# Optimization experiments

Hardware: AMD Instinct MI355X
Metric: run time of the kernel (lower is better)

Reference implementation:

```python
import jax, jax.numpy as jnp
import numpy as np

DIM = 256
HEADS = 8
HEAD_DIM = DIM // HEADS
WS = 7            # window size
SHIFT = 3         # shift size
H = 56
W = 56
B = 32
WA = WS * WS      # window area = 49
NWH, NWW = H // WS, W // WS
NW = NWH * NWW    # windows per image


def _make_attn_mask():
    # replicate the torch mask construction for the shifted windows
    img = np.zeros((H, W), dtype=np.float32)
    cnt = 0
    for hs in (slice(0, -WS), slice(-WS, -SHIFT), slice(-SHIFT, None)):
        for ws_ in (slice(0, -WS), slice(-WS, -SHIFT), slice(-SHIFT, None)):
            img[hs, ws_] = cnt
            cnt += 1
    mw = img.reshape(NWH, WS, NWW, WS).transpose(0, 2, 1, 3).reshape(-1, WA)  # (nW, 49)
    diff = mw[:, None, :] - mw[:, :, None]                                    # (nW, 49, 49)
    return np.where(diff != 0, -100.0, 0.0).astype(np.float32)


def _make_rel_index():
    coords = np.stack(np.meshgrid(np.arange(WS), np.arange(WS), indexing='ij')).reshape(2, -1)
    rel = coords[:, :, None] - coords[:, None, :]        # (2, 49, 49)
    rel = rel.transpose(1, 2, 0) + (WS - 1)              # shift to >= 0
    rel[..., 0] *= 2 * WS - 1
    return rel.sum(-1).astype(np.int32)                  # (49, 49) in [0, 169)


def setup_inputs() -> dict:
    key = jax.random.key(0)
    ks = jax.random.split(key, 12)
    s = 0.02
    inp = {
        'x': jax.random.normal(ks[0], (B, H, W, DIM), dtype=jnp.float32),
        'ln1_w': jnp.ones((DIM,), jnp.float32), 'ln1_b': jnp.zeros((DIM,), jnp.float32),
        'qkv_w': s * jax.random.normal(ks[1], (3 * DIM, DIM), jnp.float32),
        'qkv_b': jnp.zeros((3 * DIM,), jnp.float32),
        'rpb_table': s * jax.random.normal(ks[2], ((2 * WS - 1) ** 2, HEADS), jnp.float32),
        'proj_w': s * jax.random.normal(ks[3], (DIM, DIM), jnp.float32),
        'proj_b': jnp.zeros((DIM,), jnp.float32),
        'ln2_w': jnp.ones((DIM,), jnp.float32), 'ln2_b': jnp.zeros((DIM,), jnp.float32),
        'fc1_w': s * jax.random.normal(ks[4], (4 * DIM, DIM), jnp.float32),
        'fc1_b': jnp.zeros((4 * DIM,), jnp.float32),
        'ln3_w': jnp.ones((4 * DIM,), jnp.float32), 'ln3_b': jnp.zeros((4 * DIM,), jnp.float32),
        'fc2_w': s * jax.random.normal(ks[5], (DIM, 4 * DIM), jnp.float32),
        'fc2_b': jnp.zeros((DIM,), jnp.float32),
        'attn_mask': jnp.asarray(_make_attn_mask()),     # (nW, 49, 49)
        'rel_index': jnp.asarray(_make_rel_index()),     # (49, 49) int32
    }
    return inp


def _ln(x, w, b, eps=1e-5):
    m = jnp.mean(x, axis=-1, keepdims=True)
    v = jnp.mean((x - m) ** 2, axis=-1, keepdims=True)
    return (x - m) * jax.lax.rsqrt(v + eps) * w + b


def reference(x, ln1_w, ln1_b, qkv_w, qkv_b, rpb_table, proj_w, proj_b,
              ln2_w, ln2_b, fc1_w, fc1_b, ln3_w, ln3_b, fc2_w, fc2_b,
              attn_mask, rel_index):
    Bn, Hn, Wn, C = x.shape
    # ---- attention branch ----
    y = _ln(x, ln1_w, ln1_b)
    sh = jnp.roll(y, (-SHIFT, -SHIFT), axis=(1, 2))
    # window partition: (B, H, W, C) -> (B*nW, 49, C)
    win = sh.reshape(Bn, NWH, WS, NWW, WS, C).transpose(0, 1, 3, 2, 4, 5).reshape(Bn * NW, WA, C)
    qkv = win @ qkv_w.T + qkv_b                              # (Bw, 49, 3C)
    qkv = qkv.reshape(Bn * NW, WA, 3, HEADS, HEAD_DIM).transpose(2, 0, 3, 1, 4)
    q, k, v = qkv[0], qkv[1], qkv[2]                         # (Bw, h, 49, d)
    scale = HEAD_DIM ** -0.5
    attn = jnp.einsum('bhqd,bhkd->bhqk', q * scale, k)       # (Bw, h, 49, 49)
    bias = rpb_table[rel_index]                              # (49, 49, h)
    attn = attn + jnp.transpose(bias, (2, 0, 1))[None]
    attn = attn.reshape(Bn, NW, HEADS, WA, WA) + attn_mask[None, :, None]
    attn = jax.nn.softmax(attn, axis=-1).reshape(Bn * NW, HEADS, WA, WA)
    out = jnp.einsum('bhqk,bhkd->bhqd', attn, v)             # (Bw, h, 49, d)
    out = out.transpose(0, 2, 1, 3).reshape(Bn * NW, WA, C)
    out = out @ proj_w.T + proj_b
    # window reverse + un-shift
    out = out.reshape(Bn, NWH, NWW, WS, WS, C).transpose(0, 1, 3, 2, 4, 5).reshape(Bn, Hn, Wn, C)
    out = jnp.roll(out, (SHIFT, SHIFT), axis=(1, 2))
    x = x + out
    # ---- MLP branch (note: extra LayerNorm inside MLP per source) ----
    z = _ln(x, ln2_w, ln2_b)
    h = jax.nn.gelu(z @ fc1_w.T + fc1_b, approximate=False)
    h = _ln(h, ln3_w, ln3_b)
    x = x + (h @ fc2_w.T + fc2_b)
    return x
```

## Files before the change

### kernel.cpp

```cpp
#include <hip/hip_runtime.h>
#include <hip/hip_bf16.h>
#include <math.h>

typedef __attribute__((ext_vector_type(8))) short bf16x8;
typedef __attribute__((ext_vector_type(4))) float f32x4;
typedef __attribute__((ext_vector_type(4))) float f4;
typedef __attribute__((ext_vector_type(8))) unsigned short us8;
typedef __attribute__((ext_vector_type(4))) unsigned short us4;
typedef unsigned short u16;
typedef unsigned int u32;

#define HEADS 8
#define SHIFT_ 3
#define HIMG 56
#define WIMG 56
#define WA 49
#define NTOK 100352
#define NPAIR 16384

static __device__ __forceinline__ float bf2f(u16 v){ return __uint_as_float(((u32)v)<<16); }
static __device__ __forceinline__ u16 f2bf(float f){
  u32 u = __float_as_uint(f);
  return (u16)((u + 0x7fffu + ((u>>16)&1u)) >> 16);
}
static __device__ __forceinline__ float wsum(float v){
  #pragma unroll
  for (int off=32; off>0; off>>=1) v += __shfl_xor(v, off, 64);
  return v;
}
static __device__ __forceinline__ void glds16(const u16* g, u16* l){
  __builtin_amdgcn_global_load_lds(
      (const __attribute__((address_space(1))) unsigned int*)g,
      (__attribute__((address_space(3))) unsigned int*)l, 16, 0, 0);
}
static __device__ __forceinline__ int tok2pix(int row){
  int bw = row / 49, t = row - bw*49;
  int b  = bw >> 6,  w = bw & 63;
  int wh = w >> 3,   ww = w & 7;
  int th = t / 7,    tw = t - th*7;
  int r = wh*7 + th + SHIFT_; if (r >= HIMG) r -= HIMG;
  int c = ww*7 + tw + SHIFT_; if (c >= WIMG) c -= WIMG;
  return (b*HIMG + r)*WIMG + c;
}
static __device__ __forceinline__ float gelu_f(float x){
  float x2 = x*x;
  float u  = x*(0.7978845608028654f + 0.0356774081363001f*x2);
  float e  = __expf(u+u);
  float th = 1.0f - 2.0f*__builtin_amdgcn_rcpf(1.0f+e);
  return 0.5f*x*(1.0f+th);
}

__global__ void zero_kernel(float* __restrict__ p){
  p[blockIdx.x*256 + threadIdx.x] = 0.f;
}

template<int C, int ISBF>
__global__ void ln_stats_kernel(const void* __restrict__ srcv, float* __restrict__ stats){
  int wave = threadIdx.x >> 6, lane = threadIdx.x & 63;
  int tok = blockIdx.x*4 + wave;
  float s=0.f, s2=0.f;
  if (ISBF == 0){
    const float* p = (const float*)srcv + (size_t)tok*C;
    #pragma unroll
    for (int i=0;i<C/256;i++){
      f4 v = *(const f4*)(p + lane*4*(C/256) + i*4);
      #pragma unroll
      for (int e=0;e<4;e++){ float f=v[e]; s+=f; s2+=f*f; }
    }
  } else {
    const u16* p = (const u16*)srcv + (size_t)tok*C;
    #pragma unroll
    for (int i=0;i<C/512;i++){
      us8 v = *(const us8*)(p + lane*8*(C/512) + i*8);
      #pragma unroll
      for (int e=0;e<8;e++){ float f=bf2f(v[e]); s+=f; s2+=f*f; }
    }
  }
  s = wsum(s); s2 = wsum(s2);
  if (lane==0){
    float mean = s/(float)C;
    float var  = s2/(float)C - mean*mean;
    stats[2*tok]   = mean;
    stats[2*tok+1] = rsqrtf(var + 1e-5f);
  }
}

__global__ void ln_apply_kernel(const float* __restrict__ src, u16* __restrict__ dst){
  int wave = threadIdx.x >> 6, lane = threadIdx.x & 63;
  int tok = blockIdx.x*4 + wave;
  const float* p = src + (size_t)tok*256;
  f4 a = *(const f4*)(p + lane*4);
  float s = a[0]+a[1]+a[2]+a[3];
  float s2 = a[0]*a[0]+a[1]*a[1]+a[2]*a[2]+a[3]*a[3];
  s = wsum(s); s2 = wsum(s2);
  float mean = s*(1.f/256.f);
  float var  = s2*(1.f/256.f) - mean*mean;
  float rstd = rsqrtf(var + 1e-5f);
  us4 o;
  #pragma unroll
  for (int e=0;e<4;e++) o[e] = f2bf((a[e]-mean)*rstd);
  *(us4*)(dst + (size_t)tok*256 + lane*4) = o;
}

__global__ void prep_weights(
    const float* __restrict__ qkv_w, const float* __restrict__ qkv_b,
    const float* __restrict__ ln1w,  const float* __restrict__ ln1b,
    const float* __restrict__ fc1_w, const float* __restrict__ fc1_b,
    const float* __restrict__ ln2w,  const float* __restrict__ ln2b,
    const float* __restrict__ fc2_w, const float* __restrict__ fc2_b,
    const float* __restrict__ ln3w,  const float* __restrict__ ln3b,
    const float* __restrict__ proj_w, const float* __restrict__ proj_b,
    u16* __restrict__ wq, float* __restrict__ bq,
    u16* __restrict__ w1, float* __restrict__ b1,
    u16* __restrict__ w2, float* __restrict__ b2,
    u16* __restrict__ wp, float* __restrict__ bp,
    float* __restrict__ cs2)
{
  int wave = threadIdx.x>>6, lane = threadIdx.x&63;
  int n = blockIdx.x*4 + wave;
  const float *W,*lw,*lb,*bs; u16* WO; float* BO; int K, row, noln, docs;
  if (n < 768)      { W=qkv_w; lw=ln1w; lb=ln1b; bs=qkv_b; WO=wq; BO=bq; K=256;  row=n;      noln=0; docs=0; }
  else if (n < 1792){ W=fc1_w; lw=ln2w; lb=ln2b; bs=fc1_b; WO=w1; BO=b1; K=256;  row=n-768;  noln=0; docs=0; }
  else if (n < 2048){ W=fc2_w; lw=ln3w; lb=ln3b; bs=fc2_b; WO=w2; BO=b2; K=1024; row=n-1792; noln=0; docs=1; }
  else              { W=proj_w; lw=nullptr; lb=nullptr; bs=proj_b; WO=wp; BO=bp; K=256; row=n-2048; noln=1; docs=0; }
  float dot = 0.f, cs = 0.f;
  for (int k=lane; k<K; k+=64){
    float wv = W[(size_t)row*K + k];
    if (noln){
      WO[(size_t)row*K + k] = f2bf(wv);
    } else {
      dot += wv * lb[k];
      u16 q = f2bf(wv * lw[k]);
      WO[(size_t)row*K + k] = q;
      cs += bf2f(q);
    }
  }
  dot = wsum(dot);
  if (docs){ cs = wsum(cs); if (lane==0) cs2[row] = cs; }
  if (lane==0) BO[row] = bs[row] + dot;
}

template<int SMODE, int EPI, int SWAP>
__global__ __launch_bounds__(256)
void gemm8(const void* __restrict__ Av, const u16* __restrict__ Bt,
           const float* __restrict__ stats, float* __restrict__ hstats,
           const float* __restrict__ biasf, const float* __restrict__ resid,
           const float* __restrict__ colsum, void* __restrict__ outv,
           int K, int NT, int CHUNK)
{
  constexpr int BM=128, BN=128, BK=64;
  __shared__ u16 smem[16384];
  u16* As = smem;
  u16* Bs = smem + 8192;
  int b = blockIdx.x;
  int linear = (b & 7)*CHUNK + (b >> 3);
  int mt = linear / NT, nt = linear - mt*NT;
  int m0 = mt*BM, n0 = nt*BN;
  int tid  = threadIdx.x;
  int lane = tid & 63, wave = tid >> 6;
  int wr = wave >> 1, wc = wave & 1;
  int lc16 = lane & 15, g = lane >> 4;
  int nsteps = K >> 6;

  const u16* asrc[4];
  const u16* bsrc[4];
  #pragma unroll
  for (int i=0;i<4;i++){
    int c = tid + i*256;
    int row = c >> 3, ch = (c & 7) ^ (row & 7);
    if (SMODE <= 1){
      int grow = (SMODE==0) ? tok2pix(m0+row) : (m0+row);
      asrc[i] = (const u16*)Av + (size_t)grow*K + ch*8;
    }
    bsrc[i] = Bt + (size_t)(n0+row)*K + ch*8;
  }
  float smean[4], srstd[4];
  if (SMODE == 3){
    #pragma unroll
    for (int i=0;i<4;i++){
      int grow = m0 + ((tid + i*256) >> 3);
      smean[i] = stats[2*grow]; srstd[i] = stats[2*grow+1];
    }
  }

  f32x4 acc[4][4];
  #pragma unroll
  for (int i=0;i<4;i++)
    #pragma unroll
    for (int j=0;j<4;j++){ acc[i][j][0]=0.f; acc[i][j][1]=0.f; acc[i][j][2]=0.f; acc[i][j][3]=0.f; }

  f4 rcurf[4][2];
  if (SMODE == 3){
    #pragma unroll
    for (int i=0;i<4;i++){
      int c = tid + i*256; int row = c>>3, ch = c&7;
      const float* ap = (const float*)Av + (size_t)(m0+row)*K + ch*8;
      rcurf[i][0] = *(const f4*)ap; rcurf[i][1] = *(const f4*)(ap+4);
    }
  }

  for (int t=0; t<nsteps; ++t){
    int kt = t << 6;
    if (SMODE <= 1){
      #pragma unroll
      for (int i=0;i<4;i++) glds16(asrc[i]+kt, As + i*2048 + wave*512);
    } else {
      #pragma unroll
      for (int i=0;i<4;i++){
        int c = tid + i*256; int row = c>>3, ch = c&7;
        us8 o;
        #pragma unroll
        for (int e=0;e<8;e++){
          float fv = rcurf[i][e>>2][e&3];
          o[e] = f2bf((fv - smean[i])*srstd[i]);
        }
        u32 byte = (u32)(row*128 + ch*16) ^ ((u32)(row&7)<<4);
        *(us8*)(As + (byte>>1)) = o;
      }
    }
    #pragma unroll
    for (int i=0;i<4;i++) glds16(bsrc[i]+kt, Bs + i*2048 + wave*512);
    __syncthreads();
    if (SMODE == 3 && t+1 < nsteps){
      int kt1 = kt + 64;
      f4 rnextf[4][2];
      #pragma unroll
      for (int i=0;i<4;i++){
        int c = tid + i*256; int row = c>>3, ch = c&7;
        const float* ap = (const float*)Av + (size_t)(m0+row)*K + kt1 + ch*8;
        rnextf[i][0] = *(const f4*)ap; rnextf[i][1] = *(const f4*)(ap+4);
      }
      #pragma unroll
      for (int kk=0; kk<2; kk++){
        bf16x8 af[4], bfr[4];
        #pragma unroll
        for (int mi=0;mi<4;mi++){
          int r = wr*64 + mi*16 + lc16;
          u32 byte = (u32)(r*128 + kk*64 + g*16) ^ ((u32)(r&7)<<4);
          af[mi] = *(const bf16x8*)(As + (byte>>1));
        }
        #pragma unroll
        for (int ni=0;ni<4;ni++){
          int r = wc*64 + ni*16 + lc16;
          u32 byte = (u32)(r*128 + kk*64 + g*16) ^ ((u32)(r&7)<<4);
          bfr[ni] = *(const bf16x8*)(Bs + (byte>>1));
        }
        #pragma unroll
        for (int mi=0;mi<4;mi++)
          #pragma unroll
          for (int ni=0;ni<4;ni++)
            acc[mi][ni] = SWAP ? __builtin_amdgcn_mfma_f32_16x16x32_bf16(bfr[ni], af[mi], acc[mi][ni], 0, 0, 0)
                               : __builtin_amdgcn_mfma_f32_16x16x32_bf16(af[mi], bfr[ni], acc[mi][ni], 0, 0, 0);
      }
      #pragma unroll
      for (int i=0;i<4;i++){ rcurf[i][0] = rnextf[i][0]; rcurf[i][1] = rnextf[i][1]; }
    } else {
      #pragma unroll
      for (int kk=0; kk<2; kk++){
        bf16x8 af[4], bfr[4];
        #pragma unroll
        for (int mi=0;mi<4;mi++){
          int r = wr*64 + mi*16 + lc16;
          u32 byte = (u32)(r*128 + kk*64 + g*16) ^ ((u32)(r&7)<<4);
          af[mi] = *(const bf16x8*)(As + (byte>>1));
        }
        #pragma unroll
        for (int ni=0;ni<4;ni++){
          int r = wc*64 + ni*16 + lc16;
          u32 byte = (u32)(r*128 + kk*64 + g*16) ^ ((u32)(r&7)<<4);
          bfr[ni] = *(const bf16x8*)(Bs + (byte>>1));
        }
        #pragma unroll
        for (int mi=0;mi<4;mi++)
          #pragma unroll
          for (int ni=0;ni<4;ni++)
            acc[mi][ni] = SWAP ? __builtin_amdgcn_mfma_f32_16x16x32_bf16(bfr[ni], af[mi], acc[mi][ni], 0, 0, 0)
                               : __builtin_amdgcn_mfma_f32_16x16x32_bf16(af[mi], bfr[ni], acc[mi][ni], 0, 0, 0);
      }
    }
    __syncthreads();
  }

  int lr = lane >> 4;
  if (EPI==0){
    u16* Cs = smem;
    #pragma unroll
    for (int mi=0;mi<4;mi++){
      #pragma unroll
      for (int ni=0;ni<4;ni++){
        int cl = wc*64 + ni*16 + lc16;
        float bv = biasf[n0 + cl];
        #pragma unroll
        for (int j=0;j<4;j++){
          int rl = wr*64 + mi*16 + lr*4 + j;
          float v = acc[mi][ni][j] + bv;
          u32 byte = (u32)(rl*256 + cl*2) ^ ((u32)(rl&7)<<4);
          Cs[byte>>1] = f2bf(v);
        }
      }
    }
    __syncthreads();
    #pragma unroll
    for (int i=0;i<8;i++){
      int c = tid + i*256;
      int rl = c>>4, c0 = (c&15)*8;
      u32 byte = (u32)(rl*256 + c0*2) ^ ((u32)(rl&7)<<4);
      us8 v = *(const us8*)(Cs + (byte>>1));
      int row = m0 + rl, col = n0 + c0;
      int which = col>>8, hh = (col>>5)&7, d0 = col&31;
      int bwi = row/49, t = row - bwi*49;
      *(us8*)((u16*)outv + ((size_t)which*NPAIR + bwi*8 + hh)*(WA*32) + t*32 + d0) = v;
    }
  } else if (EPI==2){
    u16* Cs = smem;
    #pragma unroll
    for (int mi=0;mi<4;mi++){
      int rl = wr*64 + mi*16 + lc16;
      float ss = 0.f, sq = 0.f;
      #pragma unroll
      for (int ni=0;ni<4;ni++){
        int cl = wc*64 + ni*16 + g*4;
        f4 bv = *(const f4*)(biasf + n0 + cl);
        us4 o;
        #pragma unroll
        for (int j=0;j<4;j++){
          float v = gelu_f(acc[mi][ni][j] + bv[j]);
          ss += v; sq += v*v;
          o[j] = f2bf(v);
        }
        u32 byte = (u32)(rl*256 + cl*2) ^ ((u32)(rl&7)<<4);
        *(us4*)(Cs + (byte>>1)) = o;
      }
      ss += __shfl_xor(ss, 16, 64); ss += __shfl_xor(ss, 32, 64);
      sq += __shfl_xor(sq, 16, 64); sq += __shfl_xor(sq, 32, 64);
      if (g==0){
        int grow = m0 + rl;
        atomicAdd(&hstats[2*grow],   ss);
        atomicAdd(&hstats[2*grow+1], sq);
      }
    }
    __syncthreads();
    #pragma unroll
    for (int i=0;i<8;i++){
      int c = tid + i*256;
      int rl = c>>4, c0 = (c&15)*8;
      u32 byte = (u32)(rl*256 + c0*2) ^ ((u32)(rl&7)<<4);
      us8 v = *(const us8*)(Cs + (byte>>1));
      int row = m0 + rl, col = n0 + c0;
      *(us8*)((u16*)outv + (size_t)row*1024 + col) = v;
    }
  } else {
    float* Cs = (float*)smem;
    #pragma unroll
    for (int hp=0; hp<2; hp++){
      if (hp) __syncthreads();
      if (wc == hp){
        #pragma unroll
        for (int mi=0;mi<4;mi++){
          float rs4[4], mr4[4];
          if (EPI==4){
            #pragma unroll
            for (int j=0;j<4;j++){
              int grow = m0 + wr*64 + mi*16 + lr*4 + j;
              float s = stats[2*grow], q = stats[2*grow+1];
              float mean = s*(1.f/1024.f);
              float var  = q*(1.f/1024.f) - mean*mean;
              rs4[j] = rsqrtf(var + 1e-5f);
              mr4[j] = mean*rs4[j];
            }
          }
          #pragma unroll
          for (int ni=0;ni<4;ni++){
            int cl = ni*16 + lc16;
            int col = n0 + hp*64 + cl;
            float bv = biasf[col];
            float cw = (EPI==4) ? colsum[col] : 0.f;
            #pragma unroll
            for (int j=0;j<4;j++){
              int rl = wr*64 + mi*16 + lr*4 + j;
              float v;
              if (EPI==4) v = acc[mi][ni][j]*rs4[j] - mr4[j]*cw + bv;
              else        v = acc[mi][ni][j] + bv;
              u32 byte = (u32)(rl*256 + cl*4) ^ ((u32)(rl&7)<<4);
              *(float*)((char*)Cs + byte) = v;
            }
          }
        }
      }
      __syncthreads();
      #pragma unroll
      for (int i=0;i<8;i++){
        int c = tid + i*256;
        int row = c>>4, ch = c&15;
        u32 byte = (u32)(row*256 + ch*16) ^ ((u32)(row&7)<<4);
        f4 v = *(const f4*)((const char*)Cs + byte);
        int grow = m0 + row, col = n0 + hp*64 + ch*4;
        size_t addr;
        if (EPI==1) addr = (size_t)tok2pix(grow)*256 + col;
        else        addr = (size_t)grow*256 + col;
        f4 rr = *(const f4*)(resid + addr);
        v += rr;
        *(f4*)((float*)outv + addr) = v;
      }
    }
  }
}

__global__ void attn_mfma_kernel(
    const u16* __restrict__ qkv,
    const float* __restrict__ rpb,
    const int* __restrict__ rel,
    const float* __restrict__ mask,
    u16* __restrict__ outb)
{
  __shared__ u16 Kls[4][64*32];
  __shared__ u16 Vt [4][32*64];
  __shared__ u16 Pls[4][64*64];
  int wave = threadIdx.x>>6, lane = threadIdx.x&63;
  int pair = blockIdx.x*4 + wave;
  int bw = pair>>3, h = pair&7, w = bw&63;
  int lc = lane&15, g = lane>>4;
  const u16* qg = qkv + (size_t)pair*(WA*32);
  const u16* kg = qg + (size_t)NPAIR*(WA*32);
  const u16* vg = qg + (size_t)2*NPAIR*(WA*32);
  u16* Kp = &Kls[wave][0];
  u16* Vp = &Vt[wave][0];
  u16* Pp = &Pls[wave][0];

  #pragma unroll
  for (int i=0;i<4;i++){
    int idx = i*64 + lane;
    int r = idx>>2, seg = idx&3;
    us8 kv, vv;
    if (r < WA){
      kv = *(const us8*)(kg + r*32 + seg*8);
      vv = *(const us8*)(vg + r*32 + seg*8);
    } else {
      #pragma unroll
      for (int e=0;e<8;e++){ kv[e]=0; vv[e]=0; }
    }
    *(us8*)(Kp + r*32 + seg*8) = kv;
    #pragma unroll
    for (int e=0;e<8;e++){
      int d = seg*8 + e;
      u32 byte = ((u32)(d*128 + r*2)) ^ ((u32)(d&7)<<4);
      Vp[byte>>1] = vv[e];
    }
  }

  bf16x8 qa[4];
  #pragma unroll
  for (int mi=0;mi<4;mi++){
    int r = mi*16 + lc;
    if (r < WA) qa[mi] = *(const bf16x8*)(qg + r*32 + g*8);
    else { bf16x8 z;
           #pragma unroll
           for (int e=0;e<8;e++) z[e]=0; qa[mi]=z; }
  }

  f32x4 acc[4][4];
  #pragma unroll
  for (int i=0;i<4;i++)
    #pragma unroll
    for (int j=0;j<4;j++){ acc[i][j][0]=0.f; acc[i][j][1]=0.f; acc[i][j][2]=0.f; acc[i][j][3]=0.f; }
  __syncthreads();
  #pragma unroll
  for (int ni=0;ni<4;ni++){
    bf16x8 kb = *(const bf16x8*)(Kp + (ni*16+lc)*32 + g*8);
    #pragma unroll
    for (int mi=0;mi<4;mi++)
      acc[mi][ni] = __builtin_amdgcn_mfma_f32_16x16x32_bf16(qa[mi], kb, acc[mi][ni], 0, 0, 0);
  }

  const float scale = 0.17677669529663689f;
  float rinv[4][4];
  #pragma unroll
  for (int mi=0;mi<4;mi++){
    #pragma unroll
    for (int jr=0;jr<4;jr++){
      int i = mi*16 + g*4 + jr;
      float sv[4];
      #pragma unroll
      for (int ni=0;ni<4;ni++){
        int j = ni*16 + lc;
        float s;
        if (i < WA && j < WA){
          s = acc[mi][ni][jr]*scale + rpb[rel[i*WA+j]*8 + h] + mask[((size_t)w*WA + i)*WA + j];
        } else s = -1e9f;
        sv[ni] = s;
      }
      float mx = fmaxf(fmaxf(sv[0],sv[1]), fmaxf(sv[2],sv[3]));
      #pragma unroll
      for (int off=1; off<16; off<<=1) mx = fmaxf(mx, __shfl_xor(mx, off, 64));
      float sum = 0.f;
      #pragma unroll
      for (int ni=0;ni<4;ni++){ sv[ni] = __expf(sv[ni]-mx); sum += sv[ni]; }
      #pragma unroll
      for (int off=1; off<16; off<<=1) sum += __shfl_xor(sum, off, 64);
      rinv[mi][jr] = __builtin_amdgcn_rcpf(sum);
      #pragma unroll
      for (int ni=0;ni<4;ni++){
        int j = ni*16 + lc;
        u32 byte = ((u32)(i*128 + j*2)) ^ ((u32)(i&7)<<4);
        Pp[byte>>1] = f2bf(sv[ni]);
      }
    }
  }

  bf16x8 vb[2][2];
  #pragma unroll
  for (int kk=0;kk<2;kk++)
    #pragma unroll
    for (int ni=0;ni<2;ni++){
      int d = ni*16 + lc;
      u32 byte = ((u32)(d*128 + kk*64 + g*16)) ^ ((u32)(d&7)<<4);
      vb[kk][ni] = *(const bf16x8*)(Vp + (byte>>1));
    }
  f32x4 aco[4][2];
  #pragma unroll
  for (int i=0;i<4;i++)
    #pragma unroll
    for (int j=0;j<2;j++){ aco[i][j][0]=0.f; aco[i][j][1]=0.f; aco[i][j][2]=0.f; aco[i][j][3]=0.f; }
  #pragma unroll
  for (int mi=0;mi<4;mi++){
    int r = mi*16 + lc;
    #pragma unroll
    for (int kk=0;kk<2;kk++){
      u32 byte = ((u32)(r*128 + kk*64 + g*16)) ^ ((u32)(r&7)<<4);
      bf16x8 pa = *(const bf16x8*)(Pp + (byte>>1));
      #pragma unroll
      for (int ni=0;ni<2;ni++)
        aco[mi][ni] = __builtin_amdgcn_mfma_f32_16x16x32_bf16(pa, vb[kk][ni], aco[mi][ni], 0, 0, 0);
    }
  }

  u16* Op = Kp;
  #pragma unroll
  for (int mi=0;mi<4;mi++){
    #pragma unroll
    for (int jr=0;jr<4;jr++){
      int i = mi*16 + g*4 + jr;
      if (i < WA){
        float rv = rinv[mi][jr];
        #pragma unroll
        for (int ni=0;ni<2;ni++)
          Op[i*32 + ni*16 + lc] = f2bf(aco[mi][ni][jr]*rv);
      }
    }
  }
  __syncthreads();
  size_t obase = (size_t)(bw*WA)*256 + h*32;
  #pragma unroll
  for (int i=0;i<4;i++){
    int c = i*64 + lane;
    if (c < WA*4){
      int t = c>>2, seg = c&3;
      *(us8*)(outb + obase + (size_t)t*256 + seg*8) = *(const us8*)(Op + t*32 + seg*8);
    }
  }
}

extern "C" void kernel_launch(void* const* d_in, const int* in_sizes, int n_in,
                              void* d_out, int out_size, void* d_ws, size_t ws_size,
                              hipStream_t stream) {
  const float* x      = (const float*)d_in[0];
  const float* ln1w   = (const float*)d_in[1];
  const float* ln1b   = (const float*)d_in[2];
  const float* qkv_w  = (const float*)d_in[3];
  const float* qkv_b  = (const float*)d_in[4];
  const float* rpb    = (const float*)d_in[5];
  const float* proj_w = (const float*)d_in[6];
  const float* proj_b = (const float*)d_in[7];
  const float* ln2w   = (const float*)d_in[8];
  const float* ln2b   = (const float*)d_in[9];
  const float* fc1_w  = (const float*)d_in[10];
  const float* fc1_b  = (const float*)d_in[11];
  const float* ln3w   = (const float*)d_in[12];
  const float* ln3b   = (const float*)d_in[13];
  const float* fc2_w  = (const float*)d_in[14];
  const float* fc2_b  = (const float*)d_in[15];
  const float* amask  = (const float*)d_in[16];
  const int*   rel    = (const int*)d_in[17];
  float* out = (float*)d_out;

  char* ws = (char*)d_ws;
  float* hstats = (float*)(ws);
  float* statsB = (float*)(ws +  802816);
  float* bq     = (float*)(ws + 1605632);
  float* b1     = (float*)(ws + 1608704);
  float* b2     = (float*)(ws + 1612800);
  float* bp     = (float*)(ws + 1613824);
  float* cs2    = (float*)(ws + 1614848);
  u16*   wq     = (u16*)  (ws + 1615872);
  u16*   w1     = (u16*)  (ws + 2009088);
  u16*   w2     = (u16*)  (ws + 2533376);
  u16*   wp     = (u16*)  (ws + 3057664);
  const size_t P0 = 3188736;
  u16*   qkvbuf = (u16*)(ws + P0);
  u16*   attno  = (u16*)(ws + P0 + 154140672);
  u16*   xb     = (u16*)(ws + P0 + 154140672);
  u16*   hbuf   = (u16*)(ws + P0);
  u16*   x1b    = (u16*)(ws + P0 + 205520896);
  const int bigws = (ws_size >= (size_t)(P0 + 205520896ull + 51380224ull));

  prep_weights<<<576,256,0,stream>>>(qkv_w,qkv_b,ln1w,ln1b, fc1_w,fc1_b,ln2w,ln2b,
                                     fc2_w,fc2_b,ln3w,ln3b, proj_w,proj_b,
                                     wq,bq, w1,b1, w2,b2, wp,bp, cs2);
  ln_apply_kernel<<<NTOK/4,256,0,stream>>>(x, xb);
  gemm8<0,0,0><<<784*6,256,0,stream>>>(xb, wq, nullptr, nullptr, bq, nullptr, nullptr, qkvbuf, 256, 6, 588);
  attn_mfma_kernel<<<NPAIR/4,256,0,stream>>>(qkvbuf, rpb, rel, amask, attno);
  gemm8<1,1,0><<<784*2,256,0,stream>>>(attno, wp, nullptr, nullptr, bp, x, nullptr, out, 256, 2, 196);
  zero_kernel<<<784,256,0,stream>>>(hstats);
  if (bigws){
    ln_apply_kernel<<<NTOK/4,256,0,stream>>>(out, x1b);
    gemm8<1,2,1><<<784*8,256,0,stream>>>(x1b, w1, nullptr, hstats, b1, nullptr, nullptr, hbuf, 256, 8, 784);
  } else {
    ln_stats_kernel<256,0><<<NTOK/4,256,0,stream>>>(out, statsB);
    gemm8<3,2,1><<<784*8,256,0,stream>>>(out, w1, statsB, hstats, b1, nullptr, nullptr, hbuf, 256, 8, 784);
  }
  gemm8<1,4,0><<<784*2,256,0,stream>>>(hbuf, w2, hstats, nullptr, b2, out, cs2, out, 1024, 2, 196);
}
```

Measured before the change: 612.4 us.

## Double-buffer GEMM LDS tiles with BK=32 to overlap global loads

The GEMM kernel's K-step drops from 64 to 32, and the freed LDS is used as two ping-pong buffers for the direct global-to-LDS loads. The next tile's load is issued before the current tile's MFMAs, and each step now has one barrier instead of two. The goal is to hide global load latency behind compute. In exchange the kernel runs twice as many iterations with fewer MFMAs per barrier, and the swizzle moves to a 4-chunk pattern that may raise LDS bank conflicts.

```diff
diff --git a/kernel.cpp b/kernel.cpp
--- a/kernel.cpp
+++ b/kernel.cpp
@@ -142,16 +142,14 @@
 
 template<int SMODE, int EPI, int SWAP>
 __global__ __launch_bounds__(256)
-void gemm8(const void* __restrict__ Av, const u16* __restrict__ Bt,
+void gemm9(const void* __restrict__ Av, const u16* __restrict__ Bt,
            const float* __restrict__ stats, float* __restrict__ hstats,
            const float* __restrict__ biasf, const float* __restrict__ resid,
            const float* __restrict__ colsum, void* __restrict__ outv,
            int K, int NT, int CHUNK)
 {
-  constexpr int BM=128, BN=128, BK=64;
+  constexpr int BM=128, BN=128, BK=32;
   __shared__ u16 smem[16384];
-  u16* As = smem;
-  u16* Bs = smem + 8192;
   int b = blockIdx.x;
   int linear = (b & 7)*CHUNK + (b >> 3);
   int mt = linear / NT, nt = linear - mt*NT;
@@ -160,25 +158,25 @@
   int lane = tid & 63, wave = tid >> 6;
   int wr = wave >> 1, wc = wave & 1;
   int lc16 = lane & 15, g = lane >> 4;
-  int nsteps = K >> 6;
-
-  const u16* asrc[4];
-  const u16* bsrc[4];
-  #pragma unroll
-  for (int i=0;i<4;i++){
+  int nsteps = K >> 5;
+
+  const u16* asrc[2];
+  const u16* bsrc[2];
+  #pragma unroll
+  for (int i=0;i<2;i++){
     int c = tid + i*256;
-    int row = c >> 3, ch = (c & 7) ^ (row & 7);
+    int row = c >> 2, ch = (c & 3) ^ (row & 3);
     if (SMODE <= 1){
       int grow = (SMODE==0) ? tok2pix(m0+row) : (m0+row);
       asrc[i] = (const u16*)Av + (size_t)grow*K + ch*8;
     }
     bsrc[i] = Bt + (size_t)(n0+row)*K + ch*8;
   }
-  float smean[4], srstd[4];
+  float smean[2], srstd[2];
   if (SMODE == 3){
     #pragma unroll
-    for (int i=0;i<4;i++){
-      int grow = m0 + ((tid + i*256) >> 3);
+    for (int i=0;i<2;i++){
+      int grow = m0 + ((tid + i*256) >> 2);
       smean[i] = stats[2*grow]; srstd[i] = stats[2*grow+1];
     }
   }
@@ -189,96 +187,99 @@
     #pragma unroll
     for (int j=0;j<4;j++){ acc[i][j][0]=0.f; acc[i][j][1]=0.f; acc[i][j][2]=0.f; acc[i][j][3]=0.f; }
 
-  f4 rcurf[4][2];
-  if (SMODE == 3){
-    #pragma unroll
-    for (int i=0;i<4;i++){
-      int c = tid + i*256; int row = c>>3, ch = c&7;
+  if (SMODE <= 1){
+    #pragma unroll
+    for (int i=0;i<2;i++) glds16(asrc[i], smem + i*2048 + wave*512);
+    #pragma unroll
+    for (int i=0;i<2;i++) glds16(bsrc[i], smem + 8192 + i*2048 + wave*512);
+    __syncthreads();
+    for (int t=0; t<nsteps; ++t){
+      int cur = t & 1, nxt = cur ^ 1;
+      if (t+1 < nsteps){
+        int kt1 = (t+1) << 5;
+        #pragma unroll
+        for (int i=0;i<2;i++) glds16(asrc[i]+kt1, smem + nxt*4096 + i*2048 + wave*512);
+        #pragma unroll
+        for (int i=0;i<2;i++) glds16(bsrc[i]+kt1, smem + 8192 + nxt*4096 + i*2048 + wave*512);
+      }
+      const u16* Ap = smem + cur*4096;
+      const u16* Bp = smem + 8192 + cur*4096;
+      bf16x8 af[4], bfr[4];
+      #pragma unroll
+      for (int mi=0;mi<4;mi++){
+        int r = wr*64 + mi*16 + lc16;
+        u32 byte = (u32)(r*64 + g*16) ^ ((u32)(r&3)<<4);
+        af[mi] = *(const bf16x8*)(Ap + (byte>>1));
+      }
+      #pragma unroll
+      for (int ni=0;ni<4;ni++){
+        int r = wc*64 + ni*16 + lc16;
+        u32 byte = (u32)(r*64 + g*16) ^ ((u32)(r&3)<<4);
+        bfr[ni] = *(const bf16x8*)(Bp + (byte>>1));
+      }
+      #pragma unroll
+      for (int mi=0;mi<4;mi++)
+        #pragma unroll
+        for (int ni=0;ni<4;ni++)
+          acc[mi][ni] = SWAP ? __builtin_amdgcn_mfma_f32_16x16x32_bf16(bfr[ni], af[mi], acc[mi][ni], 0, 0, 0)
+                             : __builtin_amdgcn_mfma_f32_16x16x32_bf16(af[mi], bfr[ni], acc[mi][ni], 0, 0, 0);
+      __syncthreads();
+    }
+  } else {
+    f4 rcurf[2][2];
+    #pragma unroll
+    for (int i=0;i<2;i++){
+      int c = tid + i*256; int row = c>>2, ch = c&3;
       const float* ap = (const float*)Av + (size_t)(m0+row)*K + ch*8;
       rcurf[i][0] = *(const f4*)ap; rcurf[i][1] = *(const f4*)(ap+4);
     }
-  }
-
-  for (int t=0; t<nsteps; ++t){
-    int kt = t << 6;
-    if (SMODE <= 1){
-      #pragma unroll
-      for (int i=0;i<4;i++) glds16(asrc[i]+kt, As + i*2048 + wave*512);
-    } else {
-      #pragma unroll
-      for (int i=0;i<4;i++){
-        int c = tid + i*256; int row = c>>3, ch = c&7;
+    for (int t=0; t<nsteps; ++t){
+      int kt = t << 5;
+      #pragma unroll
+      for (int i=0;i<2;i++){
+        int c = tid + i*256; int row = c>>2, k8 = (c&3)*8;
         us8 o;
         #pragma unroll
         for (int e=0;e<8;e++){
           float fv = rcurf[i][e>>2][e&3];
           o[e] = f2bf((fv - smean[i])*srstd[i]);
         }
-        u32 byte = (u32)(row*128 + ch*16) ^ ((u32)(row&7)<<4);
-        *(us8*)(As + (byte>>1)) = o;
-      }
-    }
-    #pragma unroll
-    for (int i=0;i<4;i++) glds16(bsrc[i]+kt, Bs + i*2048 + wave*512);
-    __syncthreads();
-    if (SMODE == 3 && t+1 < nsteps){
-      int kt1 = kt + 64;
-      f4 rnextf[4][2];
-      #pragma unroll
-      for (int i=0;i<4;i++){
-        int c = tid + i*256; int row = c>>3, ch = c&7;
-        const float* ap = (const float*)Av + (size_t)(m0+row)*K + kt1 + ch*8;
-        rnextf[i][0] = *(const f4*)ap; rnextf[i][1] = *(const f4*)(ap+4);
-      }
-      #pragma unroll
-      for (int kk=0; kk<2; kk++){
-        bf16x8 af[4], bfr[4];
-        #pragma unroll
-        for (int mi=0;mi<4;mi++){
-          int r = wr*64 + mi*16 + lc16;
-          u32 byte = (u32)(r*128 + kk*64 + g*16) ^ ((u32)(r&7)<<4);
-          af[mi] = *(const bf16x8*)(As + (byte>>1));
+        u32 byte = (u32)(row*64 + k8*2) ^ ((u32)(row&3)<<4);
+        *(us8*)(smem + (byte>>1)) = o;
+      }
+      #pragma unroll
+      for (int i=0;i<2;i++) glds16(bsrc[i]+kt, smem + 8192 + i*2048 + wave*512);
+      __syncthreads();
+      if (t+1 < nsteps){
+        int kt1 = kt + 32;
+        #pragma unroll
+        for (int i=0;i<2;i++){
+          int c = tid + i*256; int row = c>>2, ch = c&3;
+          const float* ap = (const float*)Av + (size_t)(m0+row)*K + kt1 + ch*8;
+          rcurf[i][0] = *(const f4*)ap; rcurf[i][1] = *(const f4*)(ap+4);
         }
-        #pragma unroll
-        for (int ni=0;ni<4;ni++){
-          int r = wc*64 + ni*16 + lc16;
-          u32 byte = (u32)(r*128 + kk*64 + g*16) ^ ((u32)(r&7)<<4);
-          bfr[ni] = *(const bf16x8*)(Bs + (byte>>1));
-        }
-        #pragma unroll
-        for (int mi=0;mi<4;mi++)
-          #pragma unroll
-          for (int ni=0;ni<4;ni++)
-            acc[mi][ni] = SWAP ? __builtin_amdgcn_mfma_f32_16x16x32_bf16(bfr[ni], af[mi], acc[mi][ni], 0, 0, 0)
-                               : __builtin_amdgcn_mfma_f32_16x16x32_bf16(af[mi], bfr[ni], acc[mi][ni], 0, 0, 0);
-      }
-      #pragma unroll
-      for (int i=0;i<4;i++){ rcurf[i][0] = rnextf[i][0]; rcurf[i][1] = rnextf[i][1]; }
-    } else {
-      #pragma unroll
-      for (int kk=0; kk<2; kk++){
-        bf16x8 af[4], bfr[4];
-        #pragma unroll
-        for (int mi=0;mi<4;mi++){
-          int r = wr*64 + mi*16 + lc16;
-          u32 byte = (u32)(r*128 + kk*64 + g*16) ^ ((u32)(r&7)<<4);
-          af[mi] = *(const bf16x8*)(As + (byte>>1));
-        }
-        #pragma unroll
-        for (int ni=0;ni<4;ni++){
-          int r = wc*64 + ni*16 + lc16;
-          u32 byte = (u32)(r*128 + kk*64 + g*16) ^ ((u32)(r&7)<<4);
-          bfr[ni] = *(const bf16x8*)(Bs + (byte>>1));
-        }
-        #pragma unroll
-        for (int mi=0;mi<4;mi++)
-          #pragma unroll
-          for (int ni=0;ni<4;ni++)
-            acc[mi][ni] = SWAP ? __builtin_amdgcn_mfma_f32_16x16x32_bf16(bfr[ni], af[mi], acc[mi][ni], 0, 0, 0)
-                               : __builtin_amdgcn_mfma_f32_16x16x32_bf16(af[mi], bfr[ni], acc[mi][ni], 0, 0, 0);
-      }
-    }
-    __syncthreads();
+      }
+      bf16x8 af[4], bfr[4];
+      #pragma unroll
+      for (int mi=0;mi<4;mi++){
+        int r = wr*64 + mi*16 + lc16;
+        u32 byte = (u32)(r*64 + g*16) ^ ((u32)(r&3)<<4);
+        af[mi] = *(const bf16x8*)(smem + (byte>>1));
+      }
+      #pragma unroll
+      for (int ni=0;ni<4;ni++){
+        int r = wc*64 + ni*16 + lc16;
+        u32 byte = (u32)(r*64 + g*16) ^ ((u32)(r&3)<<4);
+        bfr[ni] = *(const bf16x8*)(smem + 8192 + (byte>>1));
+      }
+      #pragma unroll
+      for (int mi=0;mi<4;mi++)
+        #pragma unroll
+        for (int ni=0;ni<4;ni++)
+          acc[mi][ni] = SWAP ? __builtin_amdgcn_mfma_f32_16x16x32_bf16(bfr[ni], af[mi], acc[mi][ni], 0, 0, 0)
+                             : __builtin_amdgcn_mfma_f32_16x16x32_bf16(af[mi], bfr[ni], acc[mi][ni], 0, 0, 0);
+      __syncthreads();
+    }
   }
 
   int lr = lane >> 4;
@@ -607,16 +608,16 @@
                                      fc2_w,fc2_b,ln3w,ln3b, proj_w,proj_b,
                                      wq,bq, w1,b1, w2,b2, wp,bp, cs2);
   ln_apply_kernel<<<NTOK/4,256,0,stream>>>(x, xb);
-  gemm8<0,0,0><<<784*6,256,0,stream>>>(xb, wq, nullptr, nullptr, bq, nullptr, nullptr, qkvbuf, 256, 6, 588);
+  gemm9<0,0,0><<<784*6,256,0,stream>>>(xb, wq, nullptr, nullptr, bq, nullptr, nullptr, qkvbuf, 256, 6, 588);
   attn_mfma_kernel<<<NPAIR/4,256,0,stream>>>(qkvbuf, rpb, rel, amask, attno);
-  gemm8<1,1,0><<<784*2,256,0,stream>>>(attno, wp, nullptr, nullptr, bp, x, nullptr, out, 256, 2, 196);
+  gemm9<1,1,0><<<784*2,256,0,stream>>>(attno, wp, nullptr, nullptr, bp, x, nullptr, out, 256, 2, 196);
   zero_kernel<<<784,256,0,stream>>>(hstats);
   if (bigws){
     ln_apply_kernel<<<NTOK/4,256,0,stream>>>(out, x1b);
-    gemm8<1,2,1><<<784*8,256,0,stream>>>(x1b, w1, nullptr, hstats, b1, nullptr, nullptr, hbuf, 256, 8, 784);
+    gemm9<1,2,1><<<784*8,256,0,stream>>>(x1b, w1, nullptr, hstats, b1, nullptr, nullptr, hbuf, 256, 8, 784);
   } else {
     ln_stats_kernel<256,0><<<NTOK/4,256,0,stream>>>(out, statsB);
-    gemm8<3,2,1><<<784*8,256,0,stream>>>(out, w1, statsB, hstats, b1, nullptr, nullptr, hbuf, 256, 8, 784);
-  }
-  gemm8<1,4,0><<<784*2,256,0,stream>>>(hbuf, w2, hstats, nullptr, b2, out, cs2, out, 1024, 2, 196);
-}
+    gemm9<3,2,1><<<784*8,256,0,stream>>>(out, w1, statsB, hstats, b1, nullptr, nullptr, hbuf, 256, 8, 784);
+  }
+  gemm9<1,4,0><<<784*2,256,0,stream>>>(hbuf, w2, hstats, nullptr, b2, out, cs2, out, 1024, 2, 196);
+}
```

Result: faster. 587.5 us (-4.1%).
